# Kernel tuning notes

Measured on AMD Instinct MI355X. Metric: run time of the kernel, lower is better.

The kernel has to match this reference:

```python
import jax, jax.numpy as jnp
import numpy as np

ORDER = 7
ALPHA = 1.0
BETA = 1.0

def _jacobi_coeffs(order, a, b):
    k1 = np.zeros(order + 1, dtype=np.float32)
    k2 = np.zeros(order + 1, dtype=np.float32)
    k3 = np.zeros(order + 1, dtype=np.float32)
    for i in range(2, order + 1):
        k1[i] = (2*i + a + b) * (2*i + a + b - 1) / (2*i * (i + a + b))
        k2[i] = (2*i + a + b - 1) * (a*a - b*b) / (2*i * (i + a + b) * (2*i + a + b - 2))
        k3[i] = (i + a - 1) * (i + b - 1) * (2*i + a + b) / (i * (i + a + b) * (2*i + a + b - 2))
    return k1, k2, k3

K1, K2, K3 = _jacobi_coeffs(ORDER, ALPHA, BETA)

def setup_inputs() -> dict:
    key = jax.random.key(0)
    kx, kc = jax.random.split(key)
    batch, input_size, output_size = 4096, 512, 512
    x = jax.random.normal(kx, (batch, input_size), dtype=jnp.float32)
    coef = jax.random.normal(kc, (output_size, input_size, ORDER + 1), dtype=jnp.float32) * 0.1
    return {"x": x, "coef": coef}

def _precompute_jacobi(x):
    # x: [B, I] -> jacobi values [B, I, order+1]
    x = jnp.tanh(x)
    p0 = jnp.ones_like(x)
    p1 = 0.5 * (ALPHA + BETA + 2.0) * x - 0.5 * (ALPHA - BETA)
    vals = [p0, p1]
    for i in range(2, ORDER + 1):
        vals.append((K1[i] * x + K2[i]) * vals[i - 1] - K3[i] * vals[i - 2])
    return jnp.stack(vals, axis=2)  # [B, I, D]

def reference(x, coef):
    jac = _precompute_jacobi(x)                 # [B, I, D]
    # sum_j over input and order dims in one contraction
    return jnp.einsum('bid,jid->bj', jac, coef)  # [B, O]
```

## Files before the change

kernel.cpp:

```cpp
#include <hip/hip_runtime.h>
#include <stdint.h>

#define BATCH 4096
#define ISZ   512
#define OSZ   512
#define KDIM  4096

#define TM 128
#define TN 128
#define BK 64
#define SPLITK 4

typedef __bf16 bf16x8 __attribute__((ext_vector_type(8)));
typedef float  f32x4  __attribute__((ext_vector_type(4)));

__device__ __forceinline__ unsigned short f2bf(float f) {
    uint32_t u = __float_as_uint(f);
    u = (u + 0x7FFFu + ((u >> 16) & 1u)) >> 16;
    return (unsigned short)u;
}

__global__ __launch_bounds__(256) void convert_bf16(
    const float* __restrict__ src, unsigned short* __restrict__ dst, int n4)
{
    int idx = blockIdx.x * 256 + threadIdx.x;
    if (idx >= n4) return;
    float4 v = reinterpret_cast<const float4*>(src)[idx];
    uint2 o;
    o.x = (uint32_t)f2bf(v.x) | ((uint32_t)f2bf(v.y) << 16);
    o.y = (uint32_t)f2bf(v.z) | ((uint32_t)f2bf(v.w) << 16);
    reinterpret_cast<uint2*>(dst)[idx] = o;
}

__global__ __launch_bounds__(256, 2) void gemm_fused(
    const float* __restrict__ X,
    const unsigned short* __restrict__ Bm,
    unsigned short* __restrict__ Cp,
    int M, int N, int K)
{
    __shared__ __align__(16) unsigned short As[2][TM * BK];
    __shared__ __align__(16) unsigned short Bs[2][TN * BK];

    const int tid  = threadIdx.x;
    const int wave = tid >> 6;
    const int lane = tid & 63;
    const int wm   = (wave >> 1) * 64;
    const int wn   = (wave & 1) * 64;

    const int    m0    = blockIdx.x * TM;
    const size_t baseB = (size_t)blockIdx.y * TN * K;
    const int kper  = K / SPLITK;
    const int kbeg  = blockIdx.z * kper;
    const int niter = kper / BK;

    f32x4 acc[4][4] = {};

    const int mrow = lane & 15;
    const int kc   = lane >> 4;

    const int xr = tid >> 1;
    const int xc = (tid & 1) * 4;

    auto stageB = [&](int k0, int buf) {
        #pragma unroll
        for (int it = 0; it < 4; ++it) {
            int s    = it * 256 + tid;
            int row  = s >> 3;
            int csrc = (s & 7) ^ (row & 7);
            const unsigned short* gB = Bm + baseB + (size_t)row * K + k0 + csrc * 8;
            unsigned short* lB = &Bs[buf][0] + (size_t)(it * 256 + wave * 64) * 8;
            __builtin_amdgcn_global_load_lds(
                (const __attribute__((address_space(1))) uint32_t*)gB,
                (__attribute__((address_space(3))) uint32_t*)lB, 16, 0, 0);
        }
    };

    auto stageA = [&](int k0, int buf) {
        const int i0 = k0 >> 3;
        float4 xv = *reinterpret_cast<const float4*>(
            X + (size_t)(m0 + xr) * ISZ + i0 + xc);
        const float xs[4] = {xv.x, xv.y, xv.z, xv.w};
        #pragma unroll
        for (int j = 0; j < 4; ++j) {
            float e  = __expf(2.0f * xs[j]);
            float t  = 1.0f - 2.0f * __builtin_amdgcn_rcpf(e + 1.0f);
            float p0 = 1.0f;
            float p1 = 2.0f * t;
            float p2 = (1.875f     * t) * p1 - 0.75f       * p0;
            float p3 = (1.8666667f * t) * p2 - 0.8f        * p1;
            float p4 = (1.875f     * t) * p3 - 0.83333333f * p2;
            float p5 = (1.8857143f * t) * p4 - 0.85714287f * p3;
            float p6 = (1.8958333f * t) * p5 - 0.875f      * p4;
            float p7 = (1.9047619f * t) * p6 - 0.88888889f * p5;
            uint4 o;
            o.x = (uint32_t)f2bf(p0) | ((uint32_t)f2bf(p1) << 16);
            o.y = (uint32_t)f2bf(p2) | ((uint32_t)f2bf(p3) << 16);
            o.z = (uint32_t)f2bf(p4) | ((uint32_t)f2bf(p5) << 16);
            o.w = (uint32_t)f2bf(p6) | ((uint32_t)f2bf(p7) << 16);
            int slot = xr * 8 + ((xc + j) ^ (xr & 7));
            *reinterpret_cast<uint4*>(&As[buf][0] + (size_t)slot * 8) = o;
        }
    };

    stageB(kbeg, 0);
    stageA(kbeg, 0);
    __syncthreads();

    for (int kt = 0; kt < niter; ++kt) {
        const int k0 = kbeg + kt * BK;
        const int p  = kt & 1;
        if (kt + 1 < niter) {
            stageB(k0 + BK, 1 - p);
            stageA(k0 + BK, 1 - p);
        }

        const unsigned short* Ap = &As[p][0];
        const unsigned short* Bp = &Bs[p][0];
        #pragma unroll
        for (int ks = 0; ks < BK; ks += 32) {
            bf16x8 aF[4], bF[4];
            const int cbase = (ks >> 3) + kc;
            #pragma unroll
            for (int mi = 0; mi < 4; ++mi) {
                int r = wm + mi * 16 + mrow;
                int slot = r * 8 + (cbase ^ (r & 7));
                aF[mi] = *reinterpret_cast<const bf16x8*>(Ap + (size_t)slot * 8);
            }
            #pragma unroll
            for (int ni = 0; ni < 4; ++ni) {
                int r = wn + ni * 16 + mrow;
                int slot = r * 8 + (cbase ^ (r & 7));
                bF[ni] = *reinterpret_cast<const bf16x8*>(Bp + (size_t)slot * 8);
            }
            #pragma unroll
            for (int mi = 0; mi < 4; ++mi)
                #pragma unroll
                for (int ni = 0; ni < 4; ++ni)
                    acc[mi][ni] = __builtin_amdgcn_mfma_f32_16x16x32_bf16(
                        aF[mi], bF[ni], acc[mi][ni], 0, 0, 0);
        }
        __syncthreads();
    }

    unsigned short* Cz = Cp + (size_t)blockIdx.z * M * N;
    const int orow = blockIdx.x * TM + wm + (lane >> 4) * 4;
    const int ocol = blockIdx.y * TN + wn + (lane & 15);
    #pragma unroll
    for (int mi = 0; mi < 4; ++mi)
        #pragma unroll
        for (int ni = 0; ni < 4; ++ni)
            #pragma unroll
            for (int r = 0; r < 4; ++r)
                Cz[(size_t)(orow + mi * 16 + r) * N + ocol + ni * 16] =
                    f2bf(acc[mi][ni][r]);
}

__global__ __launch_bounds__(256) void reduce_k(
    const unsigned short* __restrict__ part, float* __restrict__ out, int n4)
{
    int idx = blockIdx.x * 256 + threadIdx.x;
    if (idx >= n4) return;
    const uint2* p = reinterpret_cast<const uint2*>(part);
    float s0 = 0.f, s1 = 0.f, s2 = 0.f, s3 = 0.f;
    #pragma unroll
    for (int z = 0; z < SPLITK; ++z) {
        uint2 v = p[(size_t)z * n4 + idx];
        s0 += __uint_as_float((v.x & 0xFFFFu) << 16);
        s1 += __uint_as_float(v.x & 0xFFFF0000u);
        s2 += __uint_as_float((v.y & 0xFFFFu) << 16);
        s3 += __uint_as_float(v.y & 0xFFFF0000u);
    }
    float4 o = {s0, s1, s2, s3};
    reinterpret_cast<float4*>(out)[idx] = o;
}

extern "C" void kernel_launch(void* const* d_in, const int* in_sizes, int n_in,
                              void* d_out, int out_size, void* d_ws, size_t ws_size,
                              hipStream_t stream)
{
    const float* x    = (const float*)d_in[0];
    const float* coef = (const float*)d_in[1];
    float* out = (float*)d_out;

    unsigned short* part  = (unsigned short*)d_ws;
    unsigned short* coefb = part + (size_t)SPLITK * BATCH * OSZ;

    int n4c = (OSZ * KDIM) / 4;
    convert_bf16<<<(n4c + 255) / 256, 256, 0, stream>>>(coef, coefb, n4c);

    dim3 grid(BATCH / TM, OSZ / TN, SPLITK);
    gemm_fused<<<grid, 256, 0, stream>>>(x, coefb, part, BATCH, OSZ, KDIM);

    int n4r = (BATCH * OSZ) / 4;
    reduce_k<<<(n4r + 255) / 256, 256, 0, stream>>>(part, out, n4r);
}
```

Measured before the change: 98.79 us.

## Load B fragments directly from global into registers, bypassing LDS

Drops the shared-memory staging of the coefficient (B) tile. Each wave now loads its own MFMA B fragments straight from global memory into registers, double-buffered in two register arrays, with the K loop unrolled by two to alternate them. This removes the LDS traffic and LDS footprint for B, but the two waves that share the same columns now each fetch the same B data, which doubles B global/L2 traffic. It also raises register pressure and gives up coalesced 16-byte tile loads.

```diff
diff --git a/kernel.cpp b/kernel.cpp
--- a/kernel.cpp
+++ b/kernel.cpp
@@ -39,7 +39,6 @@
     int M, int N, int K)
 {
     __shared__ __align__(16) unsigned short As[2][TM * BK];
-    __shared__ __align__(16) unsigned short Bs[2][TN * BK];
 
     const int tid  = threadIdx.x;
     const int wave = tid >> 6;
@@ -47,8 +46,8 @@
     const int wm   = (wave >> 1) * 64;
     const int wn   = (wave & 1) * 64;
 
-    const int    m0    = blockIdx.x * TM;
-    const size_t baseB = (size_t)blockIdx.y * TN * K;
+    const int m0 = blockIdx.x * TM;
+    const int n0 = blockIdx.y * TN;
     const int kper  = K / SPLITK;
     const int kbeg  = blockIdx.z * kper;
     const int niter = kper / BK;
@@ -61,18 +60,18 @@
     const int xr = tid >> 1;
     const int xc = (tid & 1) * 4;
 
-    auto stageB = [&](int k0, int buf) {
+    const unsigned short* browp[4];
+    #pragma unroll
+    for (int ni = 0; ni < 4; ++ni)
+        browp[ni] = Bm + (size_t)(n0 + wn + ni * 16 + mrow) * K + kc * 8;
+
+    auto loadB = [&](int k0, bf16x8 (&dst)[8]) {
         #pragma unroll
-        for (int it = 0; it < 4; ++it) {
-            int s    = it * 256 + tid;
-            int row  = s >> 3;
-            int csrc = (s & 7) ^ (row & 7);
-            const unsigned short* gB = Bm + baseB + (size_t)row * K + k0 + csrc * 8;
-            unsigned short* lB = &Bs[buf][0] + (size_t)(it * 256 + wave * 64) * 8;
-            __builtin_amdgcn_global_load_lds(
-                (const __attribute__((address_space(1))) uint32_t*)gB,
-                (__attribute__((address_space(3))) uint32_t*)lB, 16, 0, 0);
-        }
+        for (int ks = 0; ks < 2; ++ks)
+            #pragma unroll
+            for (int ni = 0; ni < 4; ++ni)
+                dst[ks * 4 + ni] = *reinterpret_cast<const bf16x8*>(
+                    browp[ni] + k0 + ks * 32);
     };
 
     auto stageA = [&](int k0, int buf) {
@@ -102,24 +101,18 @@
         }
     };
 
-    stageB(kbeg, 0);
-    stageA(kbeg, 0);
-    __syncthreads();
-
-    for (int kt = 0; kt < niter; ++kt) {
+    auto mfmaIter = [&](int kt, bf16x8 (&cur)[8], bf16x8 (&nxt)[8]) {
         const int k0 = kbeg + kt * BK;
         const int p  = kt & 1;
         if (kt + 1 < niter) {
-            stageB(k0 + BK, 1 - p);
+            loadB(k0 + BK, nxt);
             stageA(k0 + BK, 1 - p);
         }
-
         const unsigned short* Ap = &As[p][0];
-        const unsigned short* Bp = &Bs[p][0];
         #pragma unroll
-        for (int ks = 0; ks < BK; ks += 32) {
-            bf16x8 aF[4], bF[4];
-            const int cbase = (ks >> 3) + kc;
+        for (int ks = 0; ks < 2; ++ks) {
+            bf16x8 aF[4];
+            const int cbase = ks * 4 + kc;
             #pragma unroll
             for (int mi = 0; mi < 4; ++mi) {
                 int r = wm + mi * 16 + mrow;
@@ -127,19 +120,23 @@
                 aF[mi] = *reinterpret_cast<const bf16x8*>(Ap + (size_t)slot * 8);
             }
             #pragma unroll
-            for (int ni = 0; ni < 4; ++ni) {
-                int r = wn + ni * 16 + mrow;
-                int slot = r * 8 + (cbase ^ (r & 7));
-                bF[ni] = *reinterpret_cast<const bf16x8*>(Bp + (size_t)slot * 8);
-            }
-            #pragma unroll
             for (int mi = 0; mi < 4; ++mi)
                 #pragma unroll
                 for (int ni = 0; ni < 4; ++ni)
                     acc[mi][ni] = __builtin_amdgcn_mfma_f32_16x16x32_bf16(
-                        aF[mi], bF[ni], acc[mi][ni], 0, 0, 0);
+                        aF[mi], cur[ks * 4 + ni], acc[mi][ni], 0, 0, 0);
         }
         __syncthreads();
+    };
+
+    bf16x8 bufA[8], bufB[8];
+    loadB(kbeg, bufA);
+    stageA(kbeg, 0);
+    __syncthreads();
+
+    for (int kt = 0; kt < niter; kt += 2) {
+        mfmaIter(kt,     bufA, bufB);
+        mfmaIter(kt + 1, bufB, bufA);
     }
 
     unsigned short* Cz = Cp + (size_t)blockIdx.z * M * N;
```

Result: slower. 111.1 us (+12.5%).
